# Kernel tuning notes

Hardware: AMD Instinct MI355X
Metric: run time of the kernel (lower is better)

## Reference

```python
import jax, jax.numpy as jnp
import numpy as np

# --- config constants (from init_kwargs) ---
ALPHA = 0.05; SIGMA = 0.2; THETA = 0.3; A = 0.02; B_PAR = 0.1; RHO = 0.5
MULT = 2.0          # config.x_range_final[1]
GAMMA = 0.5         # power-utility exponent: u(x,r)=r*x^g/g, ux=r*x^(g-1)
N_STEPS = 100; T_FINAL = 1.0; DT = T_FINAL / N_STEPS
HID = 64; BATCH = 16384
PEN_SCALE = 100.0; LOWER = 1e-6


def _mlp(W1, b1, W2, b2, W3, b3, s):
    # tiny FeedForwardSubNet: 3 -> HID -> HID -> 1, tanh activations
    h = jnp.tanh(s @ W1 + b1)
    h = jnp.tanh(h @ W2 + b2)
    return h @ W3 + b3


def _penalise(v):
    # penalise_range(v, lower): quadratic hinge below `lower`
    return PEN_SCALE * jnp.square(jnp.maximum(LOWER - v, 0.0))


def setup_inputs() -> dict:
    key = jax.random.key(0)
    ks = jax.random.split(key, 16)
    dw = jax.random.normal(ks[0], (BATCH, 1, N_STEPS), dtype=jnp.float32) * float(np.sqrt(DT))
    X0 = jnp.ones((1,), jnp.float32)
    R0 = jnp.ones((1,), jnp.float32)
    def w(k, shape, fan):
        return jax.random.normal(k, shape, jnp.float32) / np.float32(np.sqrt(fan))
    inp = {"dw": dw, "X0": X0, "R0": R0,
           "pW1": w(ks[1], (3, HID), 3), "pb1": jnp.zeros((HID,), jnp.float32),
           "pW2": w(ks[2], (HID, HID), HID), "pb2": jnp.zeros((HID,), jnp.float32),
           "pW3": w(ks[3], (HID, 1), HID), "pb3": jnp.zeros((1,), jnp.float32),
           "qW1": w(ks[4], (3, HID), 3), "qb1": jnp.zeros((HID,), jnp.float32),
           "qW2": w(ks[5], (HID, HID), HID), "qb2": jnp.zeros((HID,), jnp.float32),
           "qW3": w(ks[6], (HID, 1), HID), "qb3": jnp.zeros((1,), jnp.float32)}
    return inp


def reference(dw, X0, R0, pW1, pb1, pW2, pb2, pW3, pb3, qW1, qb1, qW2, qb2, qW3, qb3):
    Bn = dw.shape[0]
    ones = jnp.ones((Bn, 1), dw.dtype)
    times = jnp.arange(N_STEPS + 1, dtype=dw.dtype) * DT   # [N+1]
    x0 = ones * X0
    R0v = ones * R0
    b_eff = float(np.sign(RHO)) * B_PAR

    # p_0 and dp_0 = d p_0 / d x (per-sample, rowwise independent net)
    def p_of_x(xx):
        st = jnp.concatenate([MULT * times[0] * ones, xx, R0v], 1)
        return _mlp(pW1, pb1, pW2, pb2, pW3, pb3, st)
    p0, p_vjp = jax.vjp(p_of_x, x0)
    (dp0,) = p_vjp(jnp.ones_like(p0))
    pi0 = _mlp(qW1, qb1, qW2, qb2, qW3, qb3,
               jnp.concatenate([MULT * times[0] * ones, x0, R0v], 1))

    dw_t = jnp.transpose(dw, (2, 0, 1))          # [N, B, 1]
    upd = jnp.arange(N_STEPS) < (N_STEPS - 1)    # pi not updated at last step

    def step(carry, inp):
        x, min_x, W, pi = carry
        dwi, t_next, u = inp
        x = x + x * ALPHA * DT + pi * SIGMA * THETA * DT + pi * SIGMA * dwi
        min_x = jnp.minimum(x, min_x)
        W = W + dwi
        Rv = R0v * jnp.exp((A - 0.5 * b_eff ** 2) * t_next + b_eff * W)
        p = p0 * jnp.exp(-(ALPHA + 0.5 * THETA ** 2) * t_next - THETA * W)
        st = jnp.concatenate([MULT * t_next * jnp.ones_like(x), x, Rv], 1)
        pi_new = _mlp(qW1, qb1, qW2, qb2, qW3, qb3, st)
        pi = jnp.where(u, pi_new, pi)
        return (x, min_x, W, pi), (x, Rv, pi, -p)

    (xf, min_x, Wf, pif), (xs, Rs, pis, dMs) = jax.lax.scan(
        step, (x0, x0, jnp.zeros_like(x0), pi0), (dw_t, times[1:], upd))

    # stacked process data, matching tf.concat-over-axis-0 ordering: [(N+1)*B, 1]
    x_all  = jnp.concatenate([x0[None], xs], 0).reshape(-1, 1)
    r_all  = jnp.concatenate([R0v[None], Rs], 0).reshape(-1, 1)
    pi_all = jnp.concatenate([pi0[None], pis], 0).reshape(-1, 1)
    dM_all = jnp.concatenate([(-p0)[None], dMs], 0).reshape(-1, 1)
    dM2_all = jnp.tile(-dp0, (N_STEPS + 1, 1))
    proc = jnp.concatenate([x_all, r_all, pi_all, dM_all, dM2_all], 1)  # [(N+1)*B, 5]

    # losses (non_concave = False branch)
    p_fin = -dMs[-1]
    R_fin = Rs[-1]
    xc = jnp.maximum(xf, LOWER)
    ux = R_fin * xc ** (GAMMA - 1.0)
    u_val = R_fin * xc ** GAMMA / GAMMA
    pen = _penalise(min_x)
    loss_p = jnp.mean(jnp.square(p_fin + ux) + pen)
    loss_pi = loss_p + jnp.mean(-u_val + pen)

    return jnp.concatenate([proc.reshape(-1), jnp.stack([loss_p, loss_pi])])
```

## Files before the change

### kernel.cpp

```cpp
#include <hip/hip_runtime.h>
#include <hip/hip_bf16.h>
#include <math.h>

#define NSTEP 100
#define BATCH 16384
#define MB 16
#define NBLK (BATCH/MB)
#define NT 256

#define C_ALPHA 0.05f
#define C_SIGMA 0.2f
#define C_THETA 0.3f
#define C_DT    0.01f
#define C_LOWER 1e-6f
#define C_PEN   100.0f
#define LOG2E   1.4426950408889634f
#define TSCALE  (2.0f * LOG2E)
#define CRT ( 0.015f * C_DT * LOG2E)
#define CRW ( 0.1f * LOG2E)
#define CPT (-0.095f * C_DT * LOG2E)
#define CPW (-0.3f * LOG2E)

#define WG_BARRIER() asm volatile("s_waitcnt lgkmcnt(0)\n\ts_barrier" ::: "memory")

typedef __attribute__((ext_vector_type(8))) short bf16x8;
typedef __attribute__((ext_vector_type(4))) float f32x4;
typedef __attribute__((ext_vector_type(4), aligned(4))) float f32x4a;

__device__ __forceinline__ float tanh_pre(float zs) {
    float e = __builtin_amdgcn_exp2f(zs);
    return 1.0f - 2.0f * __builtin_amdgcn_rcpf(e + 1.0f);
}
__device__ __forceinline__ unsigned f2bf_u(float f) {
    unsigned u = __float_as_uint(f);
    return (u + 0x7FFFu + ((u >> 16) & 1u)) >> 16;
}
__device__ __forceinline__ unsigned pack_bf16(float a, float b) {
    union { __hip_bfloat162 h; unsigned u; } cv;
    cv.h = __float22bfloat162_rn(make_float2(a, b));
    return cv.u;
}
__device__ __forceinline__ float dpp_row_sum16(float v) {
    int t;
    t = __builtin_amdgcn_update_dpp(0, __float_as_int(v), 0x128, 0xF, 0xF, true);
    v += __int_as_float(t);
    t = __builtin_amdgcn_update_dpp(0, __float_as_int(v), 0x124, 0xF, 0xF, true);
    v += __int_as_float(t);
    t = __builtin_amdgcn_update_dpp(0, __float_as_int(v), 0x122, 0xF, 0xF, true);
    v += __int_as_float(t);
    t = __builtin_amdgcn_update_dpp(0, __float_as_int(v), 0x121, 0xF, 0xF, true);
    v += __int_as_float(t);
    return v;
}

__global__ __launch_bounds__(NT, 4) void fused_kernel(
        const float* __restrict__ dw, const float* __restrict__ X0,
        const float* __restrict__ R0,
        const float* __restrict__ pW1, const float* __restrict__ pb1,
        const float* __restrict__ pW2, const float* __restrict__ pb2,
        const float* __restrict__ pW3, const float* __restrict__ pb3,
        const float* __restrict__ qW1, const float* __restrict__ qb1,
        const float* __restrict__ qW2, const float* __restrict__ qb2,
        const float* __restrict__ qW3, const float* __restrict__ qb3,
        float* __restrict__ ws, float* __restrict__ out) {
    __shared__ __align__(16) unsigned short sW2T[64 * 72];
    __shared__ __align__(16) float sdw[MB * NSTEP];
    __shared__ __align__(16) uint2 sA2[2][2][64][2];
    __shared__ __align__(16) float sP[2][4][16];

    const int tid = threadIdx.x;
    const int lane = tid & 63;
    const int wv = tid >> 6;
    const int ks_own = wv >> 1;
    const int half = wv & 1;
    const int b0 = blockIdx.x * MB;
    const int l15 = lane & 15, quad = lane >> 4;

    {
        const float4* g = (const float4*)(dw + (size_t)b0 * NSTEP);
        float4* s = (float4*)sdw;
        for (int u = tid; u < MB * NSTEP / 4; u += NT) s[u] = g[u];
    }
    for (int u = tid; u < 4096; u += NT) {
        int k = u >> 6, n = u & 63;
        sW2T[n * 72 + k] = (unsigned short)f2bf_u(qW2[u] * TSCALE);
    }
    __syncthreads();

    bf16x8 Bf0, Bf1;
    {
        const unsigned short* r = &sW2T[(wv * 16 + l15) * 72 + quad * 8];
        Bf0 = *(const bf16x8*)r;
        Bf1 = *(const bf16x8*)(r + 32);
    }
    float tco[4], w1xs[4], w1rs[4], b1s[4];
    {
        const int kb = ks_own * 32 + quad * 8 + half * 4;
        #pragma unroll
        for (int j = 0; j < 4; j++) {
            tco[j]  = qW1[kb + j] * (2.0f * C_DT * TSCALE);
            w1xs[j] = qW1[64 + kb + j] * TSCALE;
            w1rs[j] = qW1[128 + kb + j] * TSCALE;
            b1s[j]  = qb1[kb + j] * TSCALE;
        }
    }
    const float b2v = qb2[wv * 16 + l15] * TSCALE;
    const float w3v = qW3[wv * 16 + l15];
    const float b3 = qb3[0];
    const float X0v = X0[0], R0s = R0[0];

    float p0, dp0;
    {
        float pre = fmaf(pW1[64 + lane], X0v, fmaf(pW1[128 + lane], R0s, pb1[lane]));
        float h1 = tanh_pre(TSCALE * pre);
        float d1 = (1.0f - h1 * h1) * pW1[64 + lane];
        float a0 = pb2[lane], a1 = 0.f, a2 = 0.f, a3 = 0.f;
        float e0 = 0.f, e1 = 0.f, e2 = 0.f, e3 = 0.f;
        for (int i2 = 0; i2 < 64; i2 += 4) {
            float w0 = pW2[(i2 + 0) * 64 + lane];
            float w1 = pW2[(i2 + 1) * 64 + lane];
            float w2 = pW2[(i2 + 2) * 64 + lane];
            float w3 = pW2[(i2 + 3) * 64 + lane];
            a0 = fmaf(__shfl(h1, i2 + 0), w0, a0); e0 = fmaf(__shfl(d1, i2 + 0), w0, e0);
            a1 = fmaf(__shfl(h1, i2 + 1), w1, a1); e1 = fmaf(__shfl(d1, i2 + 1), w1, e1);
            a2 = fmaf(__shfl(h1, i2 + 2), w2, a2); e2 = fmaf(__shfl(d1, i2 + 2), w2, e2);
            a3 = fmaf(__shfl(h1, i2 + 3), w3, a3); e3 = fmaf(__shfl(d1, i2 + 3), w3, e3);
        }
        float pre2 = (a0 + a1) + (a2 + a3);
        float dpre2 = (e0 + e1) + (e2 + e3);
        float h2 = tanh_pre(TSCALE * pre2);
        float d2 = (1.0f - h2 * h2) * dpre2;
        float c1 = h2 * pW3[lane], c2 = d2 * pW3[lane];
        #pragma unroll
        for (int o = 1; o < 64; o <<= 1) {
            c1 += __shfl_xor(c1, o);
            c2 += __shfl_xor(c2, o);
        }
        p0 = c1 + pb3[0]; dp0 = c2;
    }
    const float mdp0 = -dp0;

    auto qnet = [&](int par, float fi, float xv, float rv) -> float {
        union { uint2 u2; unsigned u[2]; } Aloc;
        {
            float z0 = fmaf(w1rs[0], rv, fmaf(w1xs[0], xv, fmaf(tco[0], fi, b1s[0])));
            float z1 = fmaf(w1rs[1], rv, fmaf(w1xs[1], xv, fmaf(tco[1], fi, b1s[1])));
            float z2 = fmaf(w1rs[2], rv, fmaf(w1xs[2], xv, fmaf(tco[2], fi, b1s[2])));
            float z3 = fmaf(w1rs[3], rv, fmaf(w1xs[3], xv, fmaf(tco[3], fi, b1s[3])));
            Aloc.u[0] = pack_bf16(tanh_pre(z0), tanh_pre(z1));
            Aloc.u[1] = pack_bf16(tanh_pre(z2), tanh_pre(z3));
        }
        sA2[par][ks_own][lane][half] = Aloc.u2;
        WG_BARRIER();
        bf16x8 A0 = *(const bf16x8*)&sA2[par][0][lane][0];
        bf16x8 A1 = *(const bf16x8*)&sA2[par][1][lane][0];
        f32x4 acc = {b2v, b2v, b2v, b2v};
        acc = __builtin_amdgcn_mfma_f32_16x16x32_bf16(A0, Bf0, acc, 0, 0, 0);
        acc = __builtin_amdgcn_mfma_f32_16x16x32_bf16(A1, Bf1, acc, 0, 0, 0);
        f32x4 part;
        #pragma unroll
        for (int r = 0; r < 4; r++)
            part[r] = dpp_row_sum16(tanh_pre(acc[r]) * w3v);
        if (l15 == 0) *(f32x4*)&sP[par][wv][quad * 4] = part;
        WG_BARRIER();
        return ((sP[par][0][l15] + sP[par][1][l15]) +
                (sP[par][2][l15] + sP[par][3][l15])) + b3;
    };

    float x = X0v, Wsum = 0.0f, minx = X0v;
    float pi = qnet(0, 0.0f, X0v, R0s);
    if (wv == 3) {
        size_t base = (size_t)(b0 + l15) * 5;
        if (quad == 0) {
            f32x4a o = {X0v, R0s, pi, -p0};
            *(f32x4a*)(out + base) = o;
        } else if (quad == 1) {
            out[base + 4] = mdp0;
        }
    }

    float dw_next = sdw[l15 * NSTEP];
    #pragma unroll 1
    for (int i = 0; i < NSTEP - 1; i++) {
        const float fi = (float)(i + 1);
        float dwv = dw_next;
        dw_next = sdw[l15 * NSTEP + i + 1];
        float t = pi * C_SIGMA;
        x = fmaf(x, 1.0f + C_ALPHA * C_DT, fmaf(t, dwv, t * (C_THETA * C_DT)));
        minx = fminf(minx, x);
        Wsum += dwv;
        float R = R0s * __builtin_amdgcn_exp2f(fmaf(CRW, Wsum, CRT * fi));
        float pin = qnet((i + 1) & 1, fi, x, R);
        if (wv == 3) {
            float pm = p0 * __builtin_amdgcn_exp2f(fmaf(CPW, Wsum, CPT * fi));
            size_t base = ((size_t)(i + 1) * BATCH + b0 + l15) * 5;
            if (quad == 0) {
                f32x4a o = {x, R, pin, -pm};
                *(f32x4a*)(out + base) = o;
            } else if (quad == 1) {
                out[base + 4] = mdp0;
            }
        }
        pi = pin;
    }

    {
        float dwv = dw_next;
        float t = pi * C_SIGMA;
        x = fmaf(x, 1.0f + C_ALPHA * C_DT, fmaf(t, dwv, t * (C_THETA * C_DT)));
        minx = fminf(minx, x);
        Wsum += dwv;
        float Rf = R0s * __builtin_amdgcn_exp2f(fmaf(CRW, Wsum, CRT * (float)NSTEP));
        float pf = p0 * __builtin_amdgcn_exp2f(fmaf(CPW, Wsum, CPT * (float)NSTEP));
        if (wv == 3) {
            size_t base = ((size_t)NSTEP * BATCH + b0 + l15) * 5;
            if (quad == 0) {
                f32x4a o = {x, Rf, pi, -pf};
                *(f32x4a*)(out + base) = o;
            } else if (quad == 1) {
                out[base + 4] = mdp0;
            }
        }
        if (wv == 0) {
            float xc = fmaxf(x, C_LOWER);
            float ux = Rf * rsqrtf(xc);
            float uval = 2.0f * Rf * sqrtf(xc);
            float d = fmaxf(C_LOWER - minx, 0.0f);
            float pen = C_PEN * d * d;
            float t1 = pf + ux;
            float v1 = dpp_row_sum16(t1 * t1 + pen);
            float v2 = dpp_row_sum16(-uval + pen);
            if (lane == 0) {
                atomicAdd(&ws[3], v1);
                atomicAdd(&ws[4], v2);
                __threadfence();
                int old = atomicAdd((int*)(ws + 5), 1);
                if (old == NBLK - 1) {
                    float lp = atomicAdd(&ws[3], 0.0f) * (1.0f / (float)BATCH);
                    float lq = atomicAdd(&ws[4], 0.0f) * (1.0f / (float)BATCH);
                    out[(size_t)(NSTEP + 1) * BATCH * 5] = lp;
                    out[(size_t)(NSTEP + 1) * BATCH * 5 + 1] = lp + lq;
                }
            }
        }
    }
}

extern "C" void kernel_launch(void* const* d_in, const int* in_sizes, int n_in,
                              void* d_out, int out_size, void* d_ws, size_t ws_size,
                              hipStream_t stream) {
    const float* dw  = (const float*)d_in[0];
    const float* X0  = (const float*)d_in[1];
    const float* R0  = (const float*)d_in[2];
    const float* pW1 = (const float*)d_in[3];
    const float* pb1 = (const float*)d_in[4];
    const float* pW2 = (const float*)d_in[5];
    const float* pb2 = (const float*)d_in[6];
    const float* pW3 = (const float*)d_in[7];
    const float* pb3 = (const float*)d_in[8];
    const float* qW1 = (const float*)d_in[9];
    const float* qb1 = (const float*)d_in[10];
    const float* qW2 = (const float*)d_in[11];
    const float* qb2 = (const float*)d_in[12];
    const float* qW3 = (const float*)d_in[13];
    const float* qb3 = (const float*)d_in[14];
    float* out = (float*)d_out;
    float* ws  = (float*)d_ws;

    hipMemsetAsync(d_ws, 0, 64, stream);
    fused_kernel<<<NBLK, NT, 0, stream>>>(dw, X0, R0, pW1, pb1, pW2, pb2, pW3, pb3,
                                          qW1, qb1, qW2, qb2, qW3, qb3, ws, out);
}
```

Baseline: 205.6 us.

## Replace tanh with LDS lookup table, swap MFMA operands, recurrent R/p updates

Builds a 1024-entry shared-memory table of tanh values and slopes, and replaces the exp/rcp tanh in both hidden layers with clamped linear interpolation from it. Inputs are rescaled and offset so they index the table directly. MFMA operands are swapped so each lane holds four outputs of one sample, which replaces four DPP row reductions with a local FMA chain plus two shuffles. R and p are now updated multiplicatively each step instead of recomputed from a cumulative Wiener sum. The risks are approximation error from the interpolation and the clamp at |z|>8, extra LDS traffic and possible bank conflicts on table gathers, and drift accumulating in the recurrent products.

```diff
diff --git a/kernel.cpp b/kernel.cpp
--- a/kernel.cpp
+++ b/kernel.cpp
@@ -21,6 +21,12 @@
 #define CPT (-0.095f * C_DT * LOG2E)
 #define CPW (-0.3f * LOG2E)
 
+#define TSC   64.0f
+#define TOFF  512.0f
+#define TMAX  1023.999f
+#define AXD   (1.0f + C_ALPHA * C_DT)
+#define SIGTHDT (C_SIGMA * C_THETA * C_DT)
+
 #define WG_BARRIER() asm volatile("s_waitcnt lgkmcnt(0)\n\ts_barrier" ::: "memory")
 
 typedef __attribute__((ext_vector_type(8))) short bf16x8;
@@ -65,6 +71,7 @@
         float* __restrict__ ws, float* __restrict__ out) {
     __shared__ __align__(16) unsigned short sW2T[64 * 72];
     __shared__ __align__(16) float sdw[MB * NSTEP];
+    __shared__ __align__(16) float2 sTab[1024];
     __shared__ __align__(16) uint2 sA2[2][2][64][2];
     __shared__ __align__(16) float sP[2][4][16];
 
@@ -81,31 +88,55 @@
         float4* s = (float4*)sdw;
         for (int u = tid; u < MB * NSTEP / 4; u += NT) s[u] = g[u];
     }
-    for (int u = tid; u < 4096; u += NT) {
-        int k = u >> 6, n = u & 63;
-        sW2T[n * 72 + k] = (unsigned short)f2bf_u(qW2[u] * TSCALE);
+    for (int u4 = tid; u4 < 1024; u4 += NT) {
+        float4 w = ((const float4*)qW2)[u4];
+        int base = u4 * 4;
+        int k = base >> 6, n = base & 63;
+        sW2T[(n + 0) * 72 + k] = (unsigned short)f2bf_u(w.x * TSC);
+        sW2T[(n + 1) * 72 + k] = (unsigned short)f2bf_u(w.y * TSC);
+        sW2T[(n + 2) * 72 + k] = (unsigned short)f2bf_u(w.z * TSC);
+        sW2T[(n + 3) * 72 + k] = (unsigned short)f2bf_u(w.w * TSC);
+    }
+    for (int u = tid; u < 1024; u += NT) {
+        float z0 = (float)u * (1.0f / TSC) - 8.0f;
+        float t0 = tanh_pre(TSCALE * z0);
+        float t1 = tanh_pre(TSCALE * (z0 + 1.0f / TSC));
+        sTab[u] = make_float2(t0, t1 - t0);
     }
     __syncthreads();
 
-    bf16x8 Bf0, Bf1;
-    {
-        const unsigned short* r = &sW2T[(wv * 16 + l15) * 72 + quad * 8];
-        Bf0 = *(const bf16x8*)r;
-        Bf1 = *(const bf16x8*)(r + 32);
+    auto tab = [&](float u) -> float {
+        float uc = __builtin_amdgcn_fmed3f(u, 0.0f, TMAX);
+        int idx = (int)uc;
+        float f = uc - (float)idx;
+        float2 e = sTab[idx];
+        return fmaf(f, e.y, e.x);
+    };
+
+    bf16x8 Bw0, Bw1;
+    {
+        const unsigned short* rp = &sW2T[(wv * 16 + l15) * 72 + quad * 8];
+        Bw0 = *(const bf16x8*)rp;
+        Bw1 = *(const bf16x8*)(rp + 32);
     }
     float tco[4], w1xs[4], w1rs[4], b1s[4];
     {
         const int kb = ks_own * 32 + quad * 8 + half * 4;
         #pragma unroll
         for (int j = 0; j < 4; j++) {
-            tco[j]  = qW1[kb + j] * (2.0f * C_DT * TSCALE);
-            w1xs[j] = qW1[64 + kb + j] * TSCALE;
-            w1rs[j] = qW1[128 + kb + j] * TSCALE;
-            b1s[j]  = qb1[kb + j] * TSCALE;
-        }
-    }
-    const float b2v = qb2[wv * 16 + l15] * TSCALE;
-    const float w3v = qW3[wv * 16 + l15];
+            tco[j]  = qW1[kb + j] * (2.0f * C_DT * TSC);
+            w1xs[j] = qW1[64 + kb + j] * TSC;
+            w1rs[j] = qW1[128 + kb + j] * TSC;
+            b1s[j]  = qb1[kb + j] * TSC + TOFF;
+        }
+    }
+    f32x4 b2w;
+    float w3w[4];
+    #pragma unroll
+    for (int r = 0; r < 4; r++) {
+        b2w[r] = qb2[wv * 16 + quad * 4 + r] * TSC + TOFF;
+        w3w[r] = qW3[wv * 16 + quad * 4 + r];
+    }
     const float b3 = qb3[0];
     const float X0v = X0[0], R0s = R0[0];
 
@@ -147,27 +178,29 @@
             float z1 = fmaf(w1rs[1], rv, fmaf(w1xs[1], xv, fmaf(tco[1], fi, b1s[1])));
             float z2 = fmaf(w1rs[2], rv, fmaf(w1xs[2], xv, fmaf(tco[2], fi, b1s[2])));
             float z3 = fmaf(w1rs[3], rv, fmaf(w1xs[3], xv, fmaf(tco[3], fi, b1s[3])));
-            Aloc.u[0] = pack_bf16(tanh_pre(z0), tanh_pre(z1));
-            Aloc.u[1] = pack_bf16(tanh_pre(z2), tanh_pre(z3));
+            Aloc.u[0] = pack_bf16(tab(z0), tab(z1));
+            Aloc.u[1] = pack_bf16(tab(z2), tab(z3));
         }
         sA2[par][ks_own][lane][half] = Aloc.u2;
         WG_BARRIER();
         bf16x8 A0 = *(const bf16x8*)&sA2[par][0][lane][0];
         bf16x8 A1 = *(const bf16x8*)&sA2[par][1][lane][0];
-        f32x4 acc = {b2v, b2v, b2v, b2v};
-        acc = __builtin_amdgcn_mfma_f32_16x16x32_bf16(A0, Bf0, acc, 0, 0, 0);
-        acc = __builtin_amdgcn_mfma_f32_16x16x32_bf16(A1, Bf1, acc, 0, 0, 0);
-        f32x4 part;
-        #pragma unroll
-        for (int r = 0; r < 4; r++)
-            part[r] = dpp_row_sum16(tanh_pre(acc[r]) * w3v);
-        if (l15 == 0) *(f32x4*)&sP[par][wv][quad * 4] = part;
+        f32x4 acc = b2w;
+        acc = __builtin_amdgcn_mfma_f32_16x16x32_bf16(Bw0, A0, acc, 0, 0, 0);
+        acc = __builtin_amdgcn_mfma_f32_16x16x32_bf16(Bw1, A1, acc, 0, 0, 0);
+        float ps = fmaf(tab(acc[0]), w3w[0],
+                   fmaf(tab(acc[1]), w3w[1],
+                   fmaf(tab(acc[2]), w3w[2], tab(acc[3]) * w3w[3])));
+        ps += __shfl_xor(ps, 16);
+        ps += __shfl_xor(ps, 32);
+        if (quad == 0) sP[par][wv][l15] = ps;
         WG_BARRIER();
         return ((sP[par][0][l15] + sP[par][1][l15]) +
                 (sP[par][2][l15] + sP[par][3][l15])) + b3;
     };
 
-    float x = X0v, Wsum = 0.0f, minx = X0v;
+    float x = X0v, minx = X0v;
+    float R = R0s, pm = p0;
     float pi = qnet(0, 0.0f, X0v, R0s);
     if (wv == 3) {
         size_t base = (size_t)(b0 + l15) * 5;
@@ -185,14 +218,13 @@
         const float fi = (float)(i + 1);
         float dwv = dw_next;
         dw_next = sdw[l15 * NSTEP + i + 1];
-        float t = pi * C_SIGMA;
-        x = fmaf(x, 1.0f + C_ALPHA * C_DT, fmaf(t, dwv, t * (C_THETA * C_DT)));
+        R  *= __builtin_amdgcn_exp2f(fmaf(CRW, dwv, CRT));
+        pm *= __builtin_amdgcn_exp2f(fmaf(CPW, dwv, CPT));
+        float sp = fmaf(dwv, C_SIGMA, SIGTHDT);
+        x = fmaf(x, AXD, pi * sp);
         minx = fminf(minx, x);
-        Wsum += dwv;
-        float R = R0s * __builtin_amdgcn_exp2f(fmaf(CRW, Wsum, CRT * fi));
         float pin = qnet((i + 1) & 1, fi, x, R);
         if (wv == 3) {
-            float pm = p0 * __builtin_amdgcn_exp2f(fmaf(CPW, Wsum, CPT * fi));
             size_t base = ((size_t)(i + 1) * BATCH + b0 + l15) * 5;
             if (quad == 0) {
                 f32x4a o = {x, R, pin, -pm};
@@ -206,12 +238,12 @@
 
     {
         float dwv = dw_next;
-        float t = pi * C_SIGMA;
-        x = fmaf(x, 1.0f + C_ALPHA * C_DT, fmaf(t, dwv, t * (C_THETA * C_DT)));
+        R  *= __builtin_amdgcn_exp2f(fmaf(CRW, dwv, CRT));
+        pm *= __builtin_amdgcn_exp2f(fmaf(CPW, dwv, CPT));
+        float sp = fmaf(dwv, C_SIGMA, SIGTHDT);
+        x = fmaf(x, AXD, pi * sp);
         minx = fminf(minx, x);
-        Wsum += dwv;
-        float Rf = R0s * __builtin_amdgcn_exp2f(fmaf(CRW, Wsum, CRT * (float)NSTEP));
-        float pf = p0 * __builtin_amdgcn_exp2f(fmaf(CPW, Wsum, CPT * (float)NSTEP));
+        float Rf = R, pf = pm;
         if (wv == 3) {
             size_t base = ((size_t)NSTEP * BATCH + b0 + l15) * 5;
             if (quad == 0) {
```

Result: faster. 197.7 us (-3.8%).
